# Optimization experiments

Measured on AMD Instinct MI355X. Metric: run time of the kernel, lower is better.

## Reference

```python
import jax, jax.numpy as jnp
import numpy as np

D_MODEL = 1024; D_STATE = 64; HEADDIM = 64; EXPAND = 2
D_INNER = EXPAND * D_MODEL            # 2048
NHEADS = D_INNER // HEADDIM           # 32
NGROUPS = 1
GN = NGROUPS * D_STATE                # 64
CONV_DIM = D_INNER + 2 * (2 * GN)     # 2304
D_IN_PROJ = 2 * D_INNER + 2 * (2 * GN) + 2 * NHEADS  # 4416
K_SP = 7; K_TP = 4; CHUNK = 256
BATCH = 2; FRAMES = 8; SPATIAL = 256; SEQLEN = SPATIAL * FRAMES  # 2048


def silu(x):
    return x * jax.nn.sigmoid(x)


def flip_frames(x, f):
    # 'b (l f) d -> b l f d' flip frame axis, flatten back
    b, L, d = x.shape
    return x.reshape(b, L // f, f, d)[:, :, ::-1, :].reshape(b, L, d)


def depthwise_conv1d(x, w, b, pad):
    # x: (N, L, C), w: (C, K) depthwise, pad=(lo,hi) -> (N, L_out, C)
    y = jax.lax.conv_general_dilated(
        jnp.transpose(x, (0, 2, 1)), w[:, None, :], (1,), [pad],
        feature_group_count=w.shape[0])
    return jnp.transpose(y + b[None, :, None], (0, 2, 1))


def setup_inputs():
    rng = np.random.default_rng(0)
    f32 = lambda *s: jnp.asarray(rng.standard_normal(s), jnp.float32)
    # dt_bias init exactly as in the torch module
    dt = np.exp(rng.random(NHEADS) * (np.log(0.1) - np.log(0.001)) + np.log(0.001))
    dt = np.clip(dt, 1e-4, None)
    inv_dt = dt + np.log(-np.expm1(-dt))
    return {
        "u": f32(BATCH, SEQLEN, D_MODEL),
        "in_proj_w": f32(D_IN_PROJ, D_MODEL) * 0.02,
        "conv_sp_w": f32(CONV_DIM, K_SP) * 0.2,
        "conv_sp_b": f32(CONV_DIM) * 0.02,
        "conv_tp_w": f32(CONV_DIM, K_TP) * 0.2,
        "conv_tp_b": f32(CONV_DIM) * 0.02,
        "dt_bias": jnp.asarray(inv_dt, jnp.float32),
        "A_log": jnp.zeros((NHEADS,), jnp.float32),
        "D": jnp.ones((NHEADS,), jnp.float32),
        "fc_D_w": f32(NHEADS, D_INNER) * 0.02,
        "norm_w": jnp.ones((D_INNER,), jnp.float32),
        "out_proj_w": f32(D_MODEL, D_INNER) * 0.02,
        "num_frames": FRAMES,
    }


def chunked_scan(xh, dt, A, Bm, Cm, sp, cs):
    # xh:(R,L,h,p) dt:(R,L,h) Bm,Cm:(R,L,n). ngroups=1.
    # seq_idx semantics: rows [0:b) one segment; rows [b:2b) reset every sp tokens.
    R, L, H, P = xh.shape
    nch = L // cs
    b = R // 2
    xch = xh.reshape(R, nch, cs, H, P)
    dtc = jnp.transpose(dt.reshape(R, nch, cs, H), (0, 1, 3, 2))   # (R,nch,h,cs)
    Bch = Bm.reshape(R, nch, cs, D_STATE)
    Cch = Cm.reshape(R, nch, cs, D_STATE)
    a = dtc * A[None, None, :, None]                               # negative logs
    cum = jnp.cumsum(a, axis=-1)                                   # inclusive
    mask = jnp.tril(jnp.ones((cs, cs), bool))
    seg = cum[..., :, None] - cum[..., None, :]                    # (R,nch,h,t,s)
    Lmat = jnp.where(mask, jnp.exp(jnp.where(mask, seg, 0.0)), 0.0)
    CB = jnp.einsum('rctn,rcsn->rcts', Cch, Bch)
    M = CB[:, :, None] * Lmat * dtc[:, :, :, None, :]
    Y_intra = jnp.einsum('rchts,rcshp->rcthp', M, xch)
    # chunk-final states and cross-chunk recurrence
    G = jnp.exp(cum[..., -1:] - cum) * dtc                         # (R,nch,h,cs)
    S_chunk = jnp.einsum('rchs,rcshp,rcsn->rchpn', G, xch, Bch)
    chunk_decay = jnp.exp(cum[..., -1])                            # (R,nch,h)
    cidx = jnp.arange(nch)
    rb = (cidx > 0) & ((cidx * cs) % sp == 0)
    resetc = jnp.concatenate([jnp.zeros((b, nch), bool),
                              jnp.broadcast_to(rb, (b, nch))], axis=0)

    def cstep(S, inp):
        dec, Sc, r = inp
        S = jnp.where(r[:, None, None, None], 0.0, S)
        prev = S
        S = dec[:, :, None, None] * S + Sc
        return S, prev

    S0 = jnp.zeros((R, H, P, D_STATE), xh.dtype)
    _, prevs = jax.lax.scan(
        cstep, S0,
        (jnp.transpose(chunk_decay, (1, 0, 2)),
         jnp.transpose(S_chunk, (1, 0, 2, 3, 4)),
         resetc.T))
    prev_states = jnp.transpose(prevs, (1, 0, 2, 3, 4))            # (R,nch,h,p,n)
    Y_inter = jnp.einsum('rcht,rctn,rchpn->rcthp', jnp.exp(cum), Cch, prev_states)
    return (Y_intra + Y_inter).reshape(R, L, H, P)


def reference(u, in_proj_w, conv_sp_w, conv_sp_b, conv_tp_w, conv_tp_b,
              dt_bias, A_log, D, fc_D_w, norm_w, out_proj_w, num_frames):
    batch, seqlen, _ = u.shape
    f = num_frames
    sp = seqlen // f
    zxbcdt = u @ in_proj_w.T
    z = zxbcdt[..., :D_INNER]
    xBC = zxbcdt[..., D_INNER:D_INNER + CONV_DIM]
    dt_raw = zxbcdt[..., D_INNER + CONV_DIM:]
    dt = jnp.concatenate([dt_raw[..., :NHEADS],
                          flip_frames(dt_raw[..., NHEADS:], f)], axis=0)
    dt = jax.nn.softplus(dt + dt_bias)                             # (2b,L,h)
    A = -jnp.exp(A_log)
    # spatial depthwise conv over spatial dim per frame ('same' pad) + SiLU
    xBC = xBC.reshape(batch, sp, f, CONV_DIM).transpose(0, 2, 1, 3).reshape(batch * f, sp, CONV_DIM)
    xBC = silu(depthwise_conv1d(xBC, conv_sp_w, conv_sp_b, (K_SP // 2, K_SP // 2)))
    # causal temporal depthwise conv over frame dim per spatial location + SiLU
    xBC = xBC.reshape(batch, f, sp, CONV_DIM).transpose(0, 2, 1, 3).reshape(batch * sp, f, CONV_DIM)
    xBC = silu(depthwise_conv1d(xBC, conv_tp_w, conv_tp_b, (K_TP - 1, 0)))
    xBC = xBC.reshape(batch, seqlen, CONV_DIM)
    x = xBC[..., :D_INNER]
    BC = xBC[..., D_INNER:]
    x_orig = x
    x2 = jnp.concatenate([x, flip_frames(x, f)], axis=0)
    BC2 = jnp.concatenate([BC[..., :2 * GN], flip_frames(BC[..., 2 * GN:], f)], axis=0)
    Bm, Cm = BC2[..., :GN], BC2[..., GN:]
    xh = x2.reshape(2 * batch, seqlen, NHEADS, HEADDIM)
    y = chunked_scan(xh, dt, A, Bm, Cm, sp, CHUNK)                 # (2b,L,h,p)
    y_fwd = y[:batch].reshape(batch, seqlen, D_INNER)
    y_rev = y[batch:].reshape(batch, sp, f, D_INNER)
    # roll-by-one with zeroed first position (fwd: token axis, rev: spatial axis)
    y_fwd = jnp.concatenate([jnp.zeros_like(y_fwd[:, :1]), y_fwd[:, :-1]], axis=1)
    y_rev = jnp.concatenate([jnp.zeros_like(y_rev[:, :1]), y_rev[:, :-1]], axis=1)
    y_rev = y_rev[:, :, ::-1, :].reshape(batch, seqlen, D_INNER)
    x_res = x_orig * jnp.repeat(x_orig @ fc_D_w.T + D, HEADDIM, axis=-1)
    y = y_fwd + y_rev + x_res
    # gated RMSNorm (norm_before_gate=True): rmsnorm(y)*w*silu(z)
    y = y * jax.lax.rsqrt(jnp.mean(jnp.square(y), axis=-1, keepdims=True) + 1e-5)
    y = y * norm_w * silu(z)
    return y @ out_proj_w.T
```

## Files before the change

kernel.cpp:

```cpp
#include <hip/hip_runtime.h>
#include <hip/hip_bf16.h>
#include <math.h>

#define D_STATE   64
#define HEADDIM   64
#define D_INNER   2048
#define NHEADS    32
#define GN        64
#define CONV_DIM  2304
#define D_IN_PROJ 4416
#define ZLD       4352
#define K_SP      7
#define K_TP      4
#define CHUNK     256
#define BATCHN    2
#define FRAMES    8
#define SPATIAL   256
#define SEQLEN    2048
#define NCH       8
#define MTOT      4096

typedef __attribute__((ext_vector_type(8))) short short8;
typedef __attribute__((ext_vector_type(8))) unsigned short ushort8v;
typedef __attribute__((ext_vector_type(4))) float floatx4;

__device__ __forceinline__ float silu_f(float x) { return x / (1.f + __expf(-x)); }
__device__ __forceinline__ int flip_l(int l) { return (l & ~7) | (7 - (l & 7)); }
__device__ __forceinline__ unsigned short f2bf(float f) {
  unsigned int u = __float_as_uint(f);
  unsigned int r = (u + 0x7fffu + ((u >> 16) & 1u)) >> 16;
  return (unsigned short)r;
}
__device__ __forceinline__ float bf2f(unsigned short s) {
  return __uint_as_float(((unsigned int)s) << 16);
}
__device__ __forceinline__ unsigned int cvtpk_bf16(float lo, float hi) {
  unsigned int r;
  asm("v_cvt_pk_bf16_f32 %0, %1, %2" : "=v"(r) : "v"(lo), "v"(hi));
  return r;
}
typedef union { short8 v; unsigned int u[4]; } s8u;
__device__ __forceinline__ void gload_lds16(const unsigned short* g, unsigned short* l) {
  __builtin_amdgcn_global_load_lds((const __attribute__((address_space(1))) void*)g,
                                   (__attribute__((address_space(3))) void*)l, 16, 0, 0);
}

__global__ __launch_bounds__(256) void cast4_bf16_kernel(const float* __restrict__ a,
                                                         unsigned short* __restrict__ oa,
                                                         int na,
                                                         const float* __restrict__ b,
                                                         unsigned short* __restrict__ ob,
                                                         int nb,
                                                         const float* __restrict__ c,
                                                         unsigned short* __restrict__ oc,
                                                         int nc,
                                                         const float* __restrict__ d,
                                                         unsigned short* __restrict__ od) {
  int bid = blockIdx.x;
  const float* in;
  unsigned short* out;
  size_t blk;
  if (bid < na)                 { in = a; out = oa; blk = bid; }
  else if (bid < na + nb)       { in = b; out = ob; blk = bid - na; }
  else if (bid < na + nb + nc)  { in = c; out = oc; blk = bid - na - nb; }
  else                          { in = d; out = od; blk = bid - na - nb - nc; }
  size_t i = (blk * 256 + threadIdx.x) * 4;
  float4 v = *(const float4*)(in + i);
  ushort4 o;
  o.x = f2bf(v.x); o.y = f2bf(v.y); o.z = f2bf(v.z); o.w = f2bf(v.w);
  *(ushort4*)(out + i) = o;
}

__global__ __launch_bounds__(256) void gemm_bk64_bf16out(
    const unsigned short* __restrict__ A, int lda,
    const unsigned short* __restrict__ B, int ldb,
    unsigned short* __restrict__ C, int ldc, int K) {
  __shared__ unsigned short As[128 * 64];
  __shared__ unsigned short Bs[128 * 64];
  const int tid = threadIdx.x;
  const int lane = tid & 63;
  const int w = tid >> 6;
  const int bid = blockIdx.x;
  const int xcd = bid & 7;
  const int rp  = bid >> 3;
  const int px  = rp % 17;
  const int py  = rp / 17;
  const int m0 = ((xcd >> 1) * 8 + py) * 128;
  const int n0 = ((xcd & 1) * 17 + px) * 128;
  const int wm = (w >> 1) * 64;
  const int wn = (w & 1) * 64;
  const int lrow = lane >> 3;
  const int lperm = lane & 7;
  floatx4 acc[4][4] = {};
  for (int k0 = 0; k0 < K; k0 += 64) {
#pragma unroll
    for (int j = 0; j < 8; ++j) {
      int g = j * 4 + w;
      if (g < 16) {
        int row = g * 8 + lrow;
        int cg = (lperm ^ (row & 7)) * 8;
        gload_lds16(A + (size_t)(m0 + row) * lda + k0 + cg, &As[g * 512]);
      } else {
        int gb = g - 16;
        int row = gb * 8 + lrow;
        int cg = (lperm ^ (row & 7)) * 8;
        gload_lds16(B + (size_t)(n0 + row) * ldb + k0 + cg, &Bs[gb * 512]);
      }
    }
    __syncthreads();
    const int fr = lane & 15;
    const int kq = (lane >> 4) * 8;
#pragma unroll
    for (int kk = 0; kk < 64; kk += 32) {
      int u = (kk + kq) >> 3;
      short8 af[4], bfr[4];
#pragma unroll
      for (int i = 0; i < 4; ++i) {
        int row = wm + i * 16 + fr;
        af[i] = *(const short8*)&As[(row * 8 + (u ^ (row & 7))) * 8];
      }
#pragma unroll
      for (int j = 0; j < 4; ++j) {
        int row = wn + j * 16 + fr;
        bfr[j] = *(const short8*)&Bs[(row * 8 + (u ^ (row & 7))) * 8];
      }
#pragma unroll
      for (int i = 0; i < 4; ++i)
#pragma unroll
        for (int j = 0; j < 4; ++j)
          acc[i][j] = __builtin_amdgcn_mfma_f32_16x16x32_bf16(af[i], bfr[j], acc[i][j], 0, 0, 0);
    }
    __syncthreads();
  }
  const int fr = lane & 15;
  const int rg = (lane >> 4) * 4;
  unsigned short* Ew = &As[w * 1024];
  const int rr = lane >> 3;
  const int c8 = (lane & 7) * 8;
#pragma unroll
  for (int i = 0; i < 4; ++i) {
#pragma unroll
    for (int q = 0; q < 4; ++q)
#pragma unroll
      for (int j = 0; j < 4; ++j)
        Ew[(rg + q) * 64 + j * 16 + fr] = f2bf(acc[i][j][q]);
    ushort8v v0 = *(const ushort8v*)&Ew[rr * 64 + c8];
    ushort8v v1 = *(const ushort8v*)&Ew[(rr + 8) * 64 + c8];
    *(ushort8v*)(C + (size_t)(m0 + wm + i * 16 + rr) * ldc + n0 + wn + c8) = v0;
    *(ushort8v*)(C + (size_t)(m0 + wm + i * 16 + rr + 8) * ldc + n0 + wn + c8) = v1;
  }
}

__global__ __launch_bounds__(256) void gemm_m64_f32(
    const unsigned short* __restrict__ A, int lda,
    const unsigned short* __restrict__ B, int ldb,
    float* __restrict__ C, int ldc, int K) {
  __shared__ unsigned short As[64 * 64];
  __shared__ unsigned short Bs[128 * 64];
  const int tid = threadIdx.x;
  const int lane = tid & 63;
  const int w = tid >> 6;
  const int bid = blockIdx.x;
  const int xcd = bid & 7;
  const int q8  = bid >> 3;
  const int rsel = q8 >> 5;
  const int rp   = q8 & 31;
  const int reg  = xcd + 8 * rsel;
  const int m0 = ((reg >> 1) * 8 + (rp >> 2)) * 64;
  const int n0 = ((reg & 1) * 4 + (rp & 3)) * 128;
  const int wm = (w >> 1) * 32;
  const int wn = (w & 1) * 64;
  const int lrow = lane >> 3;
  const int lperm = lane & 7;
  floatx4 acc[2][4] = {};
  for (int k0 = 0; k0 < K; k0 += 64) {
#pragma unroll
    for (int j = 0; j < 6; ++j) {
      int g = j * 4 + w;
      if (g < 8) {
        int row = g * 8 + lrow;
        int cg = (lperm ^ (row & 7)) * 8;
        gload_lds16(A + (size_t)(m0 + row) * lda + k0 + cg, &As[g * 512]);
      } else {
        int gb = g - 8;
        int row = gb * 8 + lrow;
        int cg = (lperm ^ (row & 7)) * 8;
        gload_lds16(B + (size_t)(n0 + row) * ldb + k0 + cg, &Bs[gb * 512]);
      }
    }
    __syncthreads();
    const int fr = lane & 15;
    const int kq = (lane >> 4) * 8;
#pragma unroll
    for (int kk = 0; kk < 64; kk += 32) {
      int u = (kk + kq) >> 3;
      short8 af[2], bfr[4];
#pragma unroll
      for (int i = 0; i < 2; ++i) {
        int row = wm + i * 16 + fr;
        af[i] = *(const short8*)&As[(row * 8 + (u ^ (row & 7))) * 8];
      }
#pragma unroll
      for (int j = 0; j < 4; ++j) {
        int row = wn + j * 16 + fr;
        bfr[j] = *(const short8*)&Bs[(row * 8 + (u ^ (row & 7))) * 8];
      }
#pragma unroll
      for (int i = 0; i < 2; ++i)
#pragma unroll
        for (int j = 0; j < 4; ++j)
          acc[i][j] = __builtin_amdgcn_mfma_f32_16x16x32_bf16(af[i], bfr[j], acc[i][j], 0, 0, 0);
    }
    __syncthreads();
  }
  const int col = lane & 15;
  const int rg = (lane >> 4) * 4;
#pragma unroll
  for (int i = 0; i < 2; ++i)
#pragma unroll
    for (int j = 0; j < 4; ++j)
#pragma unroll
      for (int r = 0; r < 4; ++r)
        C[(size_t)(m0 + wm + i * 16 + rg + r) * ldc + (n0 + wn + j * 16 + col)] = acc[i][j][r];
}

__device__ __forceinline__ void ts_body_bf16(const unsigned short* __restrict__ A, int lda,
                                             const unsigned short* __restrict__ B, int ldb,
                                             float* __restrict__ C, int ldc, int N, int K,
                                             int m0, float* red) {
  const int tid = threadIdx.x;
  const int lane = tid & 63;
  const int w = tid >> 6;
  const int fr = lane & 15;
  const int kq = (lane >> 4) * 8;
  const int nt = N >> 4;
  const int kseg = K >> 2;
  const int k0 = w * kseg;
  floatx4 acc[4] = {};
  for (int k = k0; k < k0 + kseg; k += 32) {
    short8 af = *(const short8*)(A + (size_t)(m0 + fr) * lda + k + kq);
    for (int j = 0; j < nt; ++j) {
      short8 bf8 = *(const short8*)(B + (size_t)(j * 16 + fr) * ldb + k + kq);
      acc[j] = __builtin_amdgcn_mfma_f32_16x16x32_bf16(af, bf8, acc[j], 0, 0, 0);
    }
  }
  const int rg = (lane >> 4) * 4;
  for (int j = 0; j < nt; ++j)
#pragma unroll
    for (int q = 0; q < 4; ++q)
      red[w * 1024 + j * 256 + (rg + q) * 16 + fr] = acc[j][q];
  __syncthreads();
  const int entries = nt * 256;
  for (int e = tid; e < entries; e += 256) {
    float s = red[e] + red[1024 + e] + red[2048 + e] + red[3072 + e];
    int j = e >> 8, idx = e & 255, row = idx >> 4, col = idx & 15;
    C[(size_t)(m0 + row) * ldc + j * 16 + col] = s;
  }
}

__global__ __launch_bounds__(256) void gemm_ts_bf16(
    const unsigned short* __restrict__ A, int lda,
    const unsigned short* __restrict__ B, int ldb,
    float* __restrict__ C, int ldc, int N, int K) {
  __shared__ float red[4 * 1024];
  ts_body_bf16(A, lda, B, ldb, C, ldc, N, K, blockIdx.x * 16, red);
}

__global__ __launch_bounds__(256) void fused_dtconv_kernel(
    const float* __restrict__ DTraw, const float* __restrict__ dt_bias,
    const float* __restrict__ A_log, float* __restrict__ DTt, float* __restrict__ CUMS,
    const unsigned short* __restrict__ Zb, const float* __restrict__ wsp,
    const float* __restrict__ bsp, const float* __restrict__ wtp,
    const float* __restrict__ btp, unsigned short* __restrict__ XTb) {
  __shared__ __align__(16) char smem[32768];
  const int tid = threadIdx.x;
  if (blockIdx.x < 1024) {
    float* sc = (float*)smem;
    int idx = blockIdx.x * 256 + tid;
    int l  = idx & 2047;
    int rh = idx >> 11;
    int h  = rh & 31;
    int r  = rh >> 5;
    int bi = r & 1;
    int ls = (r < 2) ? l : flip_l(l);
    int ch = (r < 2) ? h : NHEADS + h;
    float raw = DTraw[((size_t)bi * SEQLEN + ls) * 64 + ch] + dt_bias[h];
    float dtv = (raw > 20.f) ? raw : log1pf(__expf(raw));
    DTt[idx] = dtv;
    float A = -__expf(A_log[h]);
    float run = dtv * A;
    sc[tid] = run;
    __syncthreads();
#pragma unroll
    for (int ofs = 1; ofs < 256; ofs <<= 1) {
      float add = (tid >= ofs) ? sc[tid - ofs] : 0.f;
      __syncthreads();
      run += add;
      sc[tid] = run;
      __syncthreads();
    }
    CUMS[idx] = run;
  } else {
    typedef float4 xsl_t[8][32];
    xsl_t* xsl = (xsl_t*)smem;
    int bid = blockIdx.x - 1024;
    const int bx = bid % 18;
    const int by = (bid / 18) & 31;
    const int bz = bid / 576;
    const int g  = tid & 31;
    const int fr = tid >> 5;
    const int c  = bx * 128 + g * 4;
    const int s0 = by * 8;
    const int bi = bz;
    float wsp_r[4][K_SP];
#pragma unroll
    for (int ch = 0; ch < 4; ++ch)
#pragma unroll
      for (int j = 0; j < K_SP; ++j) wsp_r[ch][j] = wsp[(c + ch) * K_SP + j];
    float4 bsp4 = *(const float4*)(bsp + c);
    float4 z[14];
#pragma unroll
    for (int i = 0; i < 14; ++i) {
      int ss = s0 - 3 + i;
      if (0 <= ss && ss < SPATIAL) {
        ushort4 v = *(const ushort4*)(Zb + ((size_t)bi * SEQLEN + (ss*8 + fr)) * ZLD + D_INNER + c);
        z[i] = make_float4(bf2f(v.x), bf2f(v.y), bf2f(v.z), bf2f(v.w));
      } else {
        z[i] = make_float4(0.f, 0.f, 0.f, 0.f);
      }
    }
#pragma unroll
    for (int so = 0; so < 8; ++so) {
      float4 a = bsp4;
#pragma unroll
      for (int j = 0; j < K_SP; ++j) {
        a.x += wsp_r[0][j] * z[so + j].x;
        a.y += wsp_r[1][j] * z[so + j].y;
        a.z += wsp_r[2][j] * z[so + j].z;
        a.w += wsp_r[3][j] * z[so + j].w;
      }
      a.x = silu_f(a.x); a.y = silu_f(a.y); a.z = silu_f(a.z); a.w = silu_f(a.w);
      xsl[fr][so][g] = a;
    }
    __syncthreads();
    float wtp_r[4][K_TP];
#pragma unroll
    for (int ch = 0; ch < 4; ++ch)
#pragma unroll
      for (int j = 0; j < K_TP; ++j) wtp_r[ch][j] = wtp[(c + ch) * K_TP + j];
    float4 btp4 = *(const float4*)(btp + c);
#pragma unroll
    for (int so = 0; so < 8; ++so) {
      float4 t = btp4;
#pragma unroll
      for (int j = 0; j < K_TP; ++j) {
        int ff = fr + j - (K_TP - 1);
        if (ff >= 0) {
          float4 xv = xsl[ff][so][g];
          t.x += wtp_r[0][j] * xv.x;
          t.y += wtp_r[1][j] * xv.y;
          t.z += wtp_r[2][j] * xv.z;
          t.w += wtp_r[3][j] * xv.w;
        }
      }
      ushort4 o;
      o.x = f2bf(silu_f(t.x)); o.y = f2bf(silu_f(t.y));
      o.z = f2bf(silu_f(t.z)); o.w = f2bf(silu_f(t.w));
      *(ushort4*)(XTb + ((size_t)bi * SEQLEN + ((s0 + so)*8 + fr)) * CONV_DIM + c) = o;
    }
  }
}

__global__ __launch_bounds__(256) void fused_post_kernel(
    const unsigned short* __restrict__ XTb, const float* __restrict__ DTt,
    const float* __restrict__ CUMS, float* __restrict__ CBs,
    float* __restrict__ SCH, const unsigned short* __restrict__ FCDWb,
    float* __restrict__ FCD) {
  __shared__ __align__(16) char smem[35840];
  const int tid = threadIdx.x;
  const int bidx = blockIdx.x;
  const int lane = tid & 63;
  const int w = tid >> 6;
  if (bidx < 512) {
    unsigned short* Xs = (unsigned short*)smem;
    unsigned short* Bsm = Xs + 64 * 136;
    float* gs = (float*)(Bsm + 64 * 136);
    int c = bidx & 7;
    int h = (bidx >> 3) & 31;
    int r = bidx >> 8;
    int bi = r;
    int rh = r * NHEADS + h;
    float cl = CUMS[(size_t)rh*SEQLEN + c*CHUNK + 255];
    gs[tid] = __expf(cl - CUMS[(size_t)rh*SEQLEN + c*CHUNK + tid]) * DTt[(size_t)rh*SEQLEN + c*CHUNK + tid];
    const int fr = lane & 15;
    const int kq = (lane >> 4) * 8;
    const int sr = tid >> 3;
    const int p0 = (tid & 7) * 8;
    const int swz = (tid & 7) << 3;
    floatx4 acc[4] = {};
    for (int half = 0; half < 2; ++half) {
      __syncthreads();
#pragma unroll
      for (int P = 0; P < 4; ++P) {
        int s = P * 32 + sr;
        int l = c*CHUNK + half*128 + s;
        const unsigned short* row = XTb + ((size_t)bi*SEQLEN + l)*CONV_DIM;
        ushort8v xv = *(const ushort8v*)(row + h*HEADDIM + p0);
        ushort8v bv = *(const ushort8v*)(row + D_INNER + p0);
        float g = gs[half*128 + s];
        int cswz = s ^ swz;
#pragma unroll
        for (int q = 0; q < 8; ++q) {
          Xs[(p0 + q) * 136 + cswz] = f2bf(g * bf2f(xv[q]));
          Bsm[(p0 + q) * 136 + cswz] = bv[q];
        }
      }
      __syncthreads();
#pragma unroll
      for (int sl = 0; sl < 4; ++sl) {
        int s0 = sl * 32;
        int Ra = w*16 + fr;
        short8 af = *(const short8*)&Xs[Ra * 136 + ((s0 + kq) ^ (((Ra >> 3) & 7) << 3))];
#pragma unroll
        for (int j = 0; j < 4; ++j) {
          int Rb = j*16 + fr;
          short8 bf8 = *(const short8*)&Bsm[Rb * 136 + ((s0 + kq) ^ (((Rb >> 3) & 7) << 3))];
          acc[j] = __builtin_amdgcn_mfma_f32_16x16x32_bf16(af, bf8, acc[j], 0, 0, 0);
        }
      }
    }
    const int col = lane & 15;
    const int rg = (lane >> 4) * 4;
    size_t base = (((size_t)r*NCH + c)*NHEADS + h) * (size_t)(HEADDIM*D_STATE);
#pragma unroll
    for (int j = 0; j < 4; ++j)
#pragma unroll
      for (int q = 0; q < 4; ++q)
        SCH[base + (size_t)(w*16 + rg + q)*D_STATE + j*16 + col] = acc[j][q];
  } else if (bidx < 832) {
    const int TT0[10] = {0,1,1,2,2,2,3,3,3,3};
    const int SS0[10] = {0,0,1,0,1,2,0,1,2,3};
    int t = bidx - 512;
    int tt = t % 10;
    int rc = t / 10;
    int c = rc & 7;
    int r = rc >> 3;
    int t0 = TT0[tt] * 64;
    int s0 = SS0[tt] * 64;
    int bi = r & 1;
    int bOff = D_INNER + ((r < 2) ? 0 : 2*GN);
    int cOff = bOff + GN;
    const int fr = lane & 15;
    const int kq = (lane >> 4) * 8;
    int Lc = c * CHUNK + t0 + w * 16 + fr;
    if (r >= 2) Lc = flip_l(Lc);
    const unsigned short* crow = XTb + ((size_t)bi*SEQLEN + Lc)*CONV_DIM + cOff;
    short8 af0 = *(const short8*)(crow + kq);
    short8 af1 = *(const short8*)(crow + 32 + kq);
    floatx4 acc[4] = {};
#pragma unroll
    for (int j = 0; j < 4; ++j) {
      int Ls = c * CHUNK + s0 + j * 16 + fr;
      if (r >= 2) Ls = flip_l(Ls);
      const unsigned short* brow = XTb + ((size_t)bi*SEQLEN + Ls)*CONV_DIM + bOff;
      short8 bf0 = *(const short8*)(brow + kq);
      short8 bf1 = *(const short8*)(brow + 32 + kq);
      acc[j] = __builtin_amdgcn_mfma_f32_16x16x32_bf16(af0, bf0, acc[j], 0, 0, 0);
      acc[j] = __builtin_amdgcn_mfma_f32_16x16x32_bf16(af1, bf1, acc[j], 0, 0, 0);
    }
    const int col = lane & 15;
    const int rg = (lane >> 4) * 4;
    size_t base = (((size_t)r*NCH + c) * CHUNK) * CHUNK;
#pragma unroll
    for (int j = 0; j < 4; ++j)
#pragma unroll
      for (int q = 0; q < 4; ++q)
        CBs[base + (size_t)(t0 + w*16 + rg + q)*CHUNK + (s0 + j*16 + col)] = acc[j][q];
  } else {
    ts_body_bf16(XTb, CONV_DIM, FCDWb, 2048, FCD, 32, 32, 2048,
                 (bidx - 832) * 16, (float*)smem);
  }
}

__global__ __launch_bounds__(256) void state_combine_kernel(const float* __restrict__ SCH,
                                                            const float* __restrict__ CUMS,
                                                            float* __restrict__ SPREV) {
  int bid = blockIdx.x;
  int pq = bid & 3;
  int h = (bid >> 2) & 31;
  int r = bid >> 7;
  int tid = threadIdx.x;
  int p = pq*16 + (tid >> 4);
  int n = (tid & 15) * 4;
  float4 S = make_float4(0.f, 0.f, 0.f, 0.f);
  for (int c = 0; c < NCH; ++c) {
    size_t off = ((((size_t)r*NCH + c)*NHEADS + h)*HEADDIM + p)*D_STATE + n;
    *(float4*)(SPREV + off) = S;
    float dec = __expf(CUMS[((size_t)r*NHEADS + h)*SEQLEN + c*CHUNK + 255]);
    float4 v = *(const float4*)(SCH + off);
    S.x = dec*S.x + v.x; S.y = dec*S.y + v.y;
    S.z = dec*S.z + v.z; S.w = dec*S.w + v.w;
  }
}

#define YS_ED(S0)                                                              \
  float edv[8];                                                                \
  { float4 e0_ = *(const float4*)&ecd[(S0) + kq];                              \
    float4 e1_ = *(const float4*)&ecd[(S0) + kq + 4];                          \
    edv[0]=e0_.x; edv[1]=e0_.y; edv[2]=e0_.z; edv[3]=e0_.w;                    \
    edv[4]=e1_.x; edv[5]=e1_.y; edv[6]=e1_.z; edv[7]=e1_.w; }

#define YS_BFR(S0)                                                             \
  short8 bfr[4];                                                               \
  _Pragma("unroll")                                                            \
  for (int j = 0; j < 4; ++j) {                                                \
    int R = j * 16 + fr;                                                       \
    bfr[j] = *(const short8*)&Xt[R * 264 + (((S0) + kq) ^ (((R >> 3) & 7) << 3))]; \
  }

#define YS_MFMA4(AF, ACCROW)                                                   \
  _Pragma("unroll")                                                            \
  for (int j = 0; j < 4; ++j)                                                  \
    ACCROW[j] = __builtin_amdgcn_mfma_f32_16x16x32_bf16(AF, bfr[j], ACCROW[j], 0, 0, 0);

#define YS_AF_NOMASK(C0, C1, E)                                                \
  { af_.u[0] = cvtpk_bf16(C0.x*(E)*edv[0], C0.y*(E)*edv[1]);                   \
    af_.u[1] = cvtpk_bf16(C0.z*(E)*edv[2], C0.w*(E)*edv[3]);                   \
    af_.u[2] = cvtpk_bf16(C1.x*(E)*edv[4], C1.y*(E)*edv[5]);                   \
    af_.u[3] = cvtpk_bf16(C1.z*(E)*edv[6], C1.w*(E)*edv[7]); }

#define YS_AF_MASK(C0, C1, E, TROW)                                            \
  { float wz[8] = {C0.x,C0.y,C0.z,C0.w,C1.x,C1.y,C1.z,C1.w};                   \
    _Pragma("unroll")                                                          \
    for (int jj = 0; jj < 8; ++jj) {                                           \
      float t_ = wz[jj]*(E)*edv[jj];                                           \
      wz[jj] = (kq + jj <= (TROW)) ? t_ : 0.f; }                               \
    af_.u[0]=cvtpk_bf16(wz[0],wz[1]); af_.u[1]=cvtpk_bf16(wz[2],wz[3]);        \
    af_.u[2]=cvtpk_bf16(wz[4],wz[5]); af_.u[3]=cvtpk_bf16(wz[6],wz[7]); }

#define YS_STRIP(KS, E2, ACC)                                                  \
  {                                                                            \
    const int t0s_ = (KS) * 32;                                                \
    const float* cbr0 = CBs + cbbase + (size_t)(t0s_ + fr) * CHUNK + kq;       \
    const float* cbr1 = cbr0 + (size_t)16 * CHUNK;                             \
    float4 a0 = *(const float4*)cbr0;                                          \
    float4 a1 = *(const float4*)(cbr0 + 4);                                    \
    float4 b0 = *(const float4*)cbr1;                                          \
    float4 b1 = *(const float4*)(cbr1 + 4);                                    \
    for (int sl = 0; sl < (KS); ++sl) {                                        \
      int s0 = sl * 32;                                                        \
      float4 na0 = *(const float4*)(cbr0 + s0 + 32);                           \
      float4 na1 = *(const float4*)(cbr0 + s0 + 36);                           \
      float4 nb0 = *(const float4*)(cbr1 + s0 + 32);                           \
      float4 nb1 = *(const float4*)(cbr1 + s0 + 36);                           \
      YS_ED(s0); YS_BFR(s0);                                                   \
      s8u af_;                                                                 \
      YS_AF_NOMASK(a0, a1, (E2)[0]);                                           \
      YS_MFMA4(af_.v, ACC[0]);                                                 \
      YS_AF_NOMASK(b0, b1, (E2)[1]);                                           \
      YS_MFMA4(af_.v, ACC[1]);                                                 \
      a0 = na0; a1 = na1; b0 = nb0; b1 = nb1;                                  \
    }                                                                          \
    {                                                                          \
      int s0 = (KS) * 32;                                                      \
      YS_ED(s0); YS_BFR(s0);                                                   \
      s8u af_;                                                                 \
      YS_AF_MASK(a0, a1, (E2)[0], fr);                                         \
      YS_MFMA4(af_.v, ACC[0]);                                                 \
      YS_AF_MASK(b0, b1, (E2)[1], 16 + fr);                                    \
      YS_MFMA4(af_.v, ACC[1]);                                                 \
    }                                                                          \
  }

#define YS_INTER(T0S, E2, ACC)                                                 \
  _Pragma("unroll")                                                            \
  for (int i = 0; i < 2; ++i) {                                                \
    int t = (T0S) + i * 16 + fr;                                               \
    const unsigned short* crow = XTb + ((size_t)bi*SEQLEN + c*CHUNK + t)*CONV_DIM + D_INNER + GN + n0 + kq; \
    ushort4 c0 = *(const ushort4*)crow;                                        \
    ushort4 c1 = *(const ushort4*)(crow + 4);                                  \
    float eI = (E2)[i];                                                        \
    s8u af_;                                                                   \
    af_.u[0] = cvtpk_bf16(bf2f(c0.x)*eI, bf2f(c0.y)*eI);                       \
    af_.u[1] = cvtpk_bf16(bf2f(c0.z)*eI, bf2f(c0.w)*eI);                       \
    af_.u[2] = cvtpk_bf16(bf2f(c1.x)*eI, bf2f(c1.y)*eI);                       \
    af_.u[3] = cvtpk_bf16(bf2f(c1.z)*eI, bf2f(c1.w)*eI);                       \
    YS_MFMA4(af_.v, ACC[i]);                                                   \
  }

#define YS_EPI(T0S, ACC)                                                       \
  _Pragma("unroll")                                                            \
  for (int i = 0; i < 2; ++i) {                                                \
    _Pragma("unroll")                                                          \
    for (int q = 0; q < 4; ++q)                                                \
      _Pragma("unroll")                                                        \
      for (int j = 0; j < 4; ++j)                                              \
        Ew[(rg + q) * 64 + j * 16 + fr] = f2bf(ACC[i][j][q]);                  \
    ushort8v v0 = *(const ushort8v*)&Ew[rr * 64 + c8];                         \
    ushort8v v1 = *(const ushort8v*)&Ew[(rr + 8) * 64 + c8];                   \
    *(ushort8v*)(Yb16 + ybase + (size_t)((T0S) + i*16 + rr) * D_INNER + c8) = v0;      \
    *(ushort8v*)(Yb16 + ybase + (size_t)((T0S) + i*16 + rr + 8) * D_INNER + c8) = v1;  \
  }

__global__ __launch_bounds__(256, 4) void yscan_kernel(const unsigned short* __restrict__ XTb,
                                                       const float* __restrict__ DTt,
                                                       const float* __restrict__ CUMS,
                                                       const float* __restrict__ CBs,
                                                       const float* __restrict__ SPREV,
                                                       unsigned short* __restrict__ Yb16) {
  __shared__ unsigned short Xt[64 * 264];
  __shared__ float cums[CHUNK];
  __shared__ float ecd[CHUNK];
  int tid = threadIdx.x;
  int lane = tid & 63;
  int w = tid >> 6;
  int id = blockIdx.x;
  int c = id & 7;
  int h = (id >> 3) & 31;
  int r = id >> 8;
  int rh = r * NHEADS + h;
  int bi = r & 1;
  {
    int sr = tid >> 3;
    int p0 = (tid & 7) * 8;
    int swz = (tid & 7) << 3;
#pragma unroll
    for (int P = 0; P < 8; ++P) {
      int s = P * 32 + sr;
      int L = c * CHUNK + s;
      if (r >= 2) L = flip_l(L);
      ushort8v v = *(const ushort8v*)(XTb + ((size_t)bi * SEQLEN + L) * CONV_DIM + h * HEADDIM + p0);
      int cswz = s ^ swz;
#pragma unroll
      for (int q = 0; q < 8; ++q)
        Xt[(p0 + q) * 264 + cswz] = v[q];
    }
    float cv = CUMS[(size_t)rh * SEQLEN + c * CHUNK + tid];
    cums[tid] = cv;
    ecd[tid] = __expf(-cv) * DTt[(size_t)rh * SEQLEN + c * CHUNK + tid];
  }
  __syncthreads();
  const int fr = lane & 15;
  const int kq = (lane >> 4) * 8;
  const int kA = w, kB = 7 - w;
  const int tA = kA * 32, tB = kB * 32;
  float eAr[2], eBr[2];
#pragma unroll
  for (int i = 0; i < 2; ++i) {
    eAr[i] = __expf(cums[tA + i * 16 + fr]);
    eBr[i] = __expf(cums[tB + i * 16 + fr]);
  }
  floatx4 accA[2][4] = {};
  floatx4 accB[2][4] = {};
  size_t cbbase = (((size_t)r * NCH + c) * CHUNK) * CHUNK;
  YS_STRIP(kA, eAr, accA);
  YS_STRIP(kB, eBr, accB);
  if (r < 2) {
    const float* spbase = SPREV + (((size_t)r*NCH + c)*NHEADS + h) * (size_t)(HEADDIM*D_STATE);
#pragma unroll
    for (int ns = 0; ns < 2; ++ns) {
      int n0 = ns * 32;
      short8 bfr[4];
#pragma unroll
      for (int j = 0; j < 4; ++j) {
        const float* sp = spbase + (size_t)(j*16 + fr)*D_STATE + n0 + kq;
        float4 s0v = *(const float4*)sp;
        float4 s1v = *(const float4*)(sp + 4);
        s8u bb;
        bb.u[0] = cvtpk_bf16(s0v.x, s0v.y);
        bb.u[1] = cvtpk_bf16(s0v.z, s0v.w);
        bb.u[2] = cvtpk_bf16(s1v.x, s1v.y);
        bb.u[3] = cvtpk_bf16(s1v.z, s1v.w);
        bfr[j] = bb.v;
      }
      YS_INTER(tA, eAr, accA);
      YS_INTER(tB, eBr, accB);
    }
  }
  __syncthreads();
  unsigned short* Ew = Xt + w * 1024;
  const int rg = (lane >> 4) * 4;
  const int rr = lane >> 3;
  const int c8 = (lane & 7) * 8;
  size_t ybase = ((size_t)r*SEQLEN + c*CHUNK)*D_INNER + h*HEADDIM;
  YS_EPI(tA, accA);
  YS_EPI(tB, accB);
}

__global__ __launch_bounds__(256) void combine_kernel(const unsigned short* __restrict__ Y,
                                                      const unsigned short* __restrict__ XTb,
                                                      const float* __restrict__ FCD,
                                                      const float* __restrict__ Dp,
                                                      const unsigned short* __restrict__ Zb,
                                                      const float* __restrict__ norm_w,
                                                      unsigned short* __restrict__ YPb) {
  __shared__ float red4[4];
  int row = blockIdx.x;
  int bi = row >> 11;
  int l = row & 2047;
  int s = l >> 3, fr = l & 7;
  int tid = threadIdx.x;
  int d0 = tid * 8;
  const unsigned short* yf = (l >= 1) ? Y + ((size_t)bi*SEQLEN + (l-1))*D_INNER + d0 : nullptr;
  const unsigned short* yr = (s >= 1) ? Y + ((size_t)(2+bi)*SEQLEN + ((s-1)*8 + (7-fr)))*D_INNER + d0 : nullptr;
  const unsigned short* xr = XTb + ((size_t)row)*CONV_DIM + d0;
  float fcv = FCD[(size_t)row*NHEADS + (d0 >> 6)] + Dp[d0 >> 6];
  ushort8v xv8 = *(const ushort8v*)xr;
  float v[8];
#pragma unroll
  for (int q = 0; q < 8; ++q) v[q] = bf2f(xv8[q]) * fcv;
  if (yf) {
    ushort8v a = *(const ushort8v*)yf;
#pragma unroll
    for (int q = 0; q < 8; ++q) v[q] += bf2f(a[q]);
  }
  if (yr) {
    ushort8v a = *(const ushort8v*)yr;
#pragma unroll
    for (int q = 0; q < 8; ++q) v[q] += bf2f(a[q]);
  }
  float ss = 0.f;
#pragma unroll
  for (int q = 0; q < 8; ++q) ss += v[q] * v[q];
#pragma unroll
  for (int d = 1; d < 64; d <<= 1) ss += __shfl_xor(ss, d, 64);
  if ((tid & 63) == 0) red4[tid >> 6] = ss;
  __syncthreads();
  float tot = red4[0] + red4[1] + red4[2] + red4[3];
  float rs = rsqrtf(tot / (float)D_INNER + 1e-5f);
  ushort8v zv8 = *(const ushort8v*)(Zb + ((size_t)row)*ZLD + d0);
  float4 nw0 = *(const float4*)(norm_w + d0);
  float4 nw1 = *(const float4*)(norm_w + d0 + 4);
  float nw[8] = {nw0.x,nw0.y,nw0.z,nw0.w,nw1.x,nw1.y,nw1.z,nw1.w};
  ushort8v o;
#pragma unroll
  for (int q = 0; q < 8; ++q)
    o[q] = f2bf(v[q] * rs * nw[q] * silu_f(bf2f(zv8[q])));
  *(ushort8v*)(YPb + (size_t)row*D_INNER + d0) = o;
}

extern "C" void kernel_launch(void* const* d_in, const int* in_sizes, int n_in,
                              void* d_out, int out_size, void* d_ws, size_t ws_size,
                              hipStream_t stream) {
  (void)in_sizes; (void)n_in; (void)out_size; (void)ws_size;
  const float* u          = (const float*)d_in[0];
  const float* in_proj_w  = (const float*)d_in[1];
  const float* conv_sp_w  = (const float*)d_in[2];
  const float* conv_sp_b  = (const float*)d_in[3];
  const float* conv_tp_w  = (const float*)d_in[4];
  const float* conv_tp_b  = (const float*)d_in[5];
  const float* dt_bias    = (const float*)d_in[6];
  const float* A_log      = (const float*)d_in[7];
  const float* Dp         = (const float*)d_in[8];
  const float* fc_D_w     = (const float*)d_in[9];
  const float* norm_w     = (const float*)d_in[10];
  const float* out_proj_w = (const float*)d_in[11];
  float* out = (float*)d_out;
  float* ws = (float*)d_ws;

  float* Z     = ws;
  float* SH    = Z     + 17825792ULL;
  float* XT    = SH    + 9437184ULL;
  float* DTt   = XT    + 9437184ULL;
  float* Yb    = DTt   + 262144ULL;
  float* SPREV = Yb    + 16777216ULL;
  float* FCD   = SPREV + 2097152ULL;
  float* DTraw = FCD   + 131072ULL;
  float* CUMS  = DTraw + 262144ULL;

  unsigned short* Zb   = (unsigned short*)Z;
  unsigned short* XTb  = (unsigned short*)XT;
  unsigned short* Yb16 = (unsigned short*)Yb;
  unsigned short* Ub   = (unsigned short*)Yb;
  unsigned short* Wb   = (unsigned short*)Yb + 4194304ULL;
  float* SCH = Yb + 8388608ULL;
  unsigned short* Wob = (unsigned short*)(Yb + 10485760ULL);
  unsigned short* FCDWb = (unsigned short*)(Yb + 11534336ULL);
  unsigned short* YPb = (unsigned short*)SH;

  cast4_bf16_kernel<<<10624, 256, 0, stream>>>(u, Ub, 4096, in_proj_w, Wb, 4416,
                                               out_proj_w, Wob, 2048, fc_D_w, FCDWb);
  gemm_bk64_bf16out<<<dim3(1088), 256, 0, stream>>>(Ub, 1024, Wb, 1024, Zb, ZLD, 1024);
  gemm_ts_bf16<<<256, 256, 0, stream>>>(Ub, 1024, Wb + 4352ULL*1024, 1024,
                                        DTraw, 64, 64, 1024);
  fused_dtconv_kernel<<<2176, 256, 0, stream>>>(DTraw, dt_bias, A_log, DTt, CUMS,
                                                Zb, conv_sp_w, conv_sp_b,
                                                conv_tp_w, conv_tp_b, XTb);
  fused_post_kernel<<<1088, 256, 0, stream>>>(XTb, DTt, CUMS, SH, SCH, FCDWb, FCD);
  state_combine_kernel<<<256, 256, 0, stream>>>(SCH, CUMS, SPREV);
  yscan_kernel<<<dim3(1024), 256, 0, stream>>>(XTb, DTt, CUMS, SH, SPREV, Yb16);
  combine_kernel<<<4096, 256, 0, stream>>>(Yb16, XTb, FCD, Dp, Zb, norm_w, YPb);
  gemm_m64_f32<<<dim3(512), 256, 0, stream>>>(YPb, 2048, Wob, 2048, out, 1024, 2048);
}
```

Measured before the change: 289.9 us.

## Fuse dt GEMM into main GEMM and inline state combine into yscan

```diff
diff --git a/kernel.cpp b/kernel.cpp
--- a/kernel.cpp
+++ b/kernel.cpp
@@ -71,15 +71,56 @@
   *(ushort4*)(out + i) = o;
 }
 
-__global__ __launch_bounds__(256) void gemm_bk64_bf16out(
-    const unsigned short* __restrict__ A, int lda,
-    const unsigned short* __restrict__ B, int ldb,
-    unsigned short* __restrict__ C, int ldc, int K) {
-  __shared__ unsigned short As[128 * 64];
-  __shared__ unsigned short Bs[128 * 64];
+__device__ __forceinline__ void ts_body_bf16(const unsigned short* __restrict__ A, int lda,
+                                             const unsigned short* __restrict__ B, int ldb,
+                                             float* __restrict__ C, int ldc, int N, int K,
+                                             int m0, float* red) {
   const int tid = threadIdx.x;
   const int lane = tid & 63;
   const int w = tid >> 6;
+  const int fr = lane & 15;
+  const int kq = (lane >> 4) * 8;
+  const int nt = N >> 4;
+  const int kseg = K >> 2;
+  const int k0 = w * kseg;
+  floatx4 acc[4] = {};
+  for (int k = k0; k < k0 + kseg; k += 32) {
+    short8 af = *(const short8*)(A + (size_t)(m0 + fr) * lda + k + kq);
+    for (int j = 0; j < nt; ++j) {
+      short8 bf8 = *(const short8*)(B + (size_t)(j * 16 + fr) * ldb + k + kq);
+      acc[j] = __builtin_amdgcn_mfma_f32_16x16x32_bf16(af, bf8, acc[j], 0, 0, 0);
+    }
+  }
+  const int rg = (lane >> 4) * 4;
+  for (int j = 0; j < nt; ++j)
+#pragma unroll
+    for (int q = 0; q < 4; ++q)
+      red[w * 1024 + j * 256 + (rg + q) * 16 + fr] = acc[j][q];
+  __syncthreads();
+  const int entries = nt * 256;
+  for (int e = tid; e < entries; e += 256) {
+    float s = red[e] + red[1024 + e] + red[2048 + e] + red[3072 + e];
+    int j = e >> 8, idx = e & 255, row = idx >> 4, col = idx & 15;
+    C[(size_t)(m0 + row) * ldc + j * 16 + col] = s;
+  }
+}
+
+__global__ __launch_bounds__(256) void gemm_main_kernel(
+    const unsigned short* __restrict__ A, int lda,
+    const unsigned short* __restrict__ B, int ldb,
+    unsigned short* __restrict__ C, int ldc, int K,
+    const unsigned short* __restrict__ Bdt, float* __restrict__ DTraw) {
+  __shared__ __align__(16) char smem[32768];
+  const int tid = threadIdx.x;
+  const int lane = tid & 63;
+  const int w = tid >> 6;
+  if (blockIdx.x >= 1088) {
+    ts_body_bf16(A, lda, Bdt, lda, DTraw, 64, 64, K,
+                 (blockIdx.x - 1088) * 16, (float*)smem);
+    return;
+  }
+  unsigned short* As = (unsigned short*)smem;
+  unsigned short* Bs = As + 128 * 64;
   const int bid = blockIdx.x;
   const int xcd = bid & 7;
   const int rp  = bid >> 3;
@@ -222,48 +263,6 @@
 #pragma unroll
       for (int r = 0; r < 4; ++r)
         C[(size_t)(m0 + wm + i * 16 + rg + r) * ldc + (n0 + wn + j * 16 + col)] = acc[i][j][r];
-}
-
-__device__ __forceinline__ void ts_body_bf16(const unsigned short* __restrict__ A, int lda,
-                                             const unsigned short* __restrict__ B, int ldb,
-                                             float* __restrict__ C, int ldc, int N, int K,
-                                             int m0, float* red) {
-  const int tid = threadIdx.x;
-  const int lane = tid & 63;
-  const int w = tid >> 6;
-  const int fr = lane & 15;
-  const int kq = (lane >> 4) * 8;
-  const int nt = N >> 4;
-  const int kseg = K >> 2;
-  const int k0 = w * kseg;
-  floatx4 acc[4] = {};
-  for (int k = k0; k < k0 + kseg; k += 32) {
-    short8 af = *(const short8*)(A + (size_t)(m0 + fr) * lda + k + kq);
-    for (int j = 0; j < nt; ++j) {
-      short8 bf8 = *(const short8*)(B + (size_t)(j * 16 + fr) * ldb + k + kq);
-      acc[j] = __builtin_amdgcn_mfma_f32_16x16x32_bf16(af, bf8, acc[j], 0, 0, 0);
-    }
-  }
-  const int rg = (lane >> 4) * 4;
-  for (int j = 0; j < nt; ++j)
-#pragma unroll
-    for (int q = 0; q < 4; ++q)
-      red[w * 1024 + j * 256 + (rg + q) * 16 + fr] = acc[j][q];
-  __syncthreads();
-  const int entries = nt * 256;
-  for (int e = tid; e < entries; e += 256) {
-    float s = red[e] + red[1024 + e] + red[2048 + e] + red[3072 + e];
-    int j = e >> 8, idx = e & 255, row = idx >> 4, col = idx & 15;
-    C[(size_t)(m0 + row) * ldc + j * 16 + col] = s;
-  }
-}
-
-__global__ __launch_bounds__(256) void gemm_ts_bf16(
-    const unsigned short* __restrict__ A, int lda,
-    const unsigned short* __restrict__ B, int ldb,
-    float* __restrict__ C, int ldc, int N, int K) {
-  __shared__ float red[4 * 1024];
-  ts_body_bf16(A, lda, B, ldb, C, ldc, N, K, blockIdx.x * 16, red);
 }
 
 __global__ __launch_bounds__(256) void fused_dtconv_kernel(
@@ -440,11 +439,11 @@
   } else if (bidx < 832) {
     const int TT0[10] = {0,1,1,2,2,2,3,3,3,3};
     const int SS0[10] = {0,0,1,0,1,2,0,1,2,3};
-    int t = bidx - 512;
-    int tt = t % 10;
-    int rc = t / 10;
-    int c = rc & 7;
-    int r = rc >> 3;
+    int idx = bidx - 512;
+    int c = idx & 7;
+    int k = idx >> 3;
+    int tt = k % 10;
+    int r = k / 10;
     int t0 = TT0[tt] * 64;
     int s0 = SS0[tt] * 64;
     int bi = r & 1;
@@ -479,27 +478,6 @@
   } else {
     ts_body_bf16(XTb, CONV_DIM, FCDWb, 2048, FCD, 32, 32, 2048,
                  (bidx - 832) * 16, (float*)smem);
-  }
-}
-
-__global__ __launch_bounds__(256) void state_combine_kernel(const float* __restrict__ SCH,
-                                                            const float* __restrict__ CUMS,
-                                                            float* __restrict__ SPREV) {
-  int bid = blockIdx.x;
-  int pq = bid & 3;
-  int h = (bid >> 2) & 31;
-  int r = bid >> 7;
-  int tid = threadIdx.x;
-  int p = pq*16 + (tid >> 4);
-  int n = (tid & 15) * 4;
-  float4 S = make_float4(0.f, 0.f, 0.f, 0.f);
-  for (int c = 0; c < NCH; ++c) {
-    size_t off = ((((size_t)r*NCH + c)*NHEADS + h)*HEADDIM + p)*D_STATE + n;
-    *(float4*)(SPREV + off) = S;
-    float dec = __expf(CUMS[((size_t)r*NHEADS + h)*SEQLEN + c*CHUNK + 255]);
-    float4 v = *(const float4*)(SCH + off);
-    S.x = dec*S.x + v.x; S.y = dec*S.y + v.y;
-    S.z = dec*S.z + v.z; S.w = dec*S.w + v.w;
   }
 }
 
@@ -606,7 +584,7 @@
                                                        const float* __restrict__ DTt,
                                                        const float* __restrict__ CUMS,
                                                        const float* __restrict__ CBs,
-                                                       const float* __restrict__ SPREV,
+                                                       const float* __restrict__ SCH,
                                                        unsigned short* __restrict__ Yb16) {
   __shared__ unsigned short Xt[64 * 264];
   __shared__ float cums[CHUNK];
@@ -653,30 +631,41 @@
   floatx4 accA[2][4] = {};
   floatx4 accB[2][4] = {};
   size_t cbbase = (((size_t)r * NCH + c) * CHUNK) * CHUNK;
+  if (r < 2) {
+#pragma unroll
+    for (int ns = 0; ns < 2; ++ns) {
+      int n0 = ns * 32;
+      float sp[4][8] = {};
+      for (int cp = 0; cp < c; ++cp) {
+        float dec = __expf(CUMS[(size_t)rh*SEQLEN + cp*CHUNK + 255]);
+        const float* sb = SCH + (((size_t)r*NCH + cp)*NHEADS + h) * (size_t)(HEADDIM*D_STATE);
+#pragma unroll
+        for (int j = 0; j < 4; ++j) {
+          const float* p = sb + (size_t)(j*16 + fr)*D_STATE + n0 + kq;
+          float4 v0 = *(const float4*)p;
+          float4 v1 = *(const float4*)(p + 4);
+          sp[j][0] = dec*sp[j][0] + v0.x; sp[j][1] = dec*sp[j][1] + v0.y;
+          sp[j][2] = dec*sp[j][2] + v0.z; sp[j][3] = dec*sp[j][3] + v0.w;
+          sp[j][4] = dec*sp[j][4] + v1.x; sp[j][5] = dec*sp[j][5] + v1.y;
+          sp[j][6] = dec*sp[j][6] + v1.z; sp[j][7] = dec*sp[j][7] + v1.w;
+        }
+      }
+      short8 bfr[4];
+#pragma unroll
+      for (int j = 0; j < 4; ++j) {
+        s8u bb;
+        bb.u[0] = cvtpk_bf16(sp[j][0], sp[j][1]);
+        bb.u[1] = cvtpk_bf16(sp[j][2], sp[j][3]);
+        bb.u[2] = cvtpk_bf16(sp[j][4], sp[j][5]);
+        bb.u[3] = cvtpk_bf16(sp[j][6], sp[j][7]);
+        bfr[j] = bb.v;
+      }
+      YS_INTER(tA, eAr, accA);
+      YS_INTER(tB, eBr, accB);
+    }
+  }
   YS_STRIP(kA, eAr, accA);
   YS_STRIP(kB, eBr, accB);
-  if (r < 2) {
-    const float* spbase = SPREV + (((size_t)r*NCH + c)*NHEADS + h) * (size_t)(HEADDIM*D_STATE);
-#pragma unroll
-    for (int ns = 0; ns < 2; ++ns) {
-      int n0 = ns * 32;
-      short8 bfr[4];
-#pragma unroll
-      for (int j = 0; j < 4; ++j) {
-        const float* sp = spbase + (size_t)(j*16 + fr)*D_STATE + n0 + kq;
-        float4 s0v = *(const float4*)sp;
-        float4 s1v = *(const float4*)(sp + 4);
-        s8u bb;
-        bb.u[0] = cvtpk_bf16(s0v.x, s0v.y);
-        bb.u[1] = cvtpk_bf16(s0v.z, s0v.w);
-        bb.u[2] = cvtpk_bf16(s1v.x, s1v.y);
-        bb.u[3] = cvtpk_bf16(s1v.z, s1v.w);
-        bfr[j] = bb.v;
-      }
-      YS_INTER(tA, eAr, accA);
-      YS_INTER(tB, eBr, accB);
-    }
-  }
   __syncthreads();
   unsigned short* Ew = Xt + w * 1024;
   const int rg = (lane >> 4) * 4;
@@ -780,15 +769,13 @@
 
   cast4_bf16_kernel<<<10624, 256, 0, stream>>>(u, Ub, 4096, in_proj_w, Wb, 4416,
                                                out_proj_w, Wob, 2048, fc_D_w, FCDWb);
-  gemm_bk64_bf16out<<<dim3(1088), 256, 0, stream>>>(Ub, 1024, Wb, 1024, Zb, ZLD, 1024);
-  gemm_ts_bf16<<<256, 256, 0, stream>>>(Ub, 1024, Wb + 4352ULL*1024, 1024,
-                                        DTraw, 64, 64, 1024);
+  gemm_main_kernel<<<dim3(1344), 256, 0, stream>>>(Ub, 1024, Wb, 1024, Zb, ZLD, 1024,
+                                                   Wb + 4352ULL*1024, DTraw);
   fused_dtconv_kernel<<<2176, 256, 0, stream>>>(DTraw, dt_bias, A_log, DTt, CUMS,
                                                 Zb, conv_sp_w, conv_sp_b,
                                                 conv_tp_w, conv_tp_b, XTb);
   fused_post_kernel<<<1088, 256, 0, stream>>>(XTb, DTt, CUMS, SH, SCH, FCDWb, FCD);
-  state_combine_kernel<<<256, 256, 0, stream>>>(SCH, CUMS, SPREV);
-  yscan_kernel<<<dim3(1024), 256, 0, stream>>>(XTb, DTt, CUMS, SH, SPREV, Yb16);
+  yscan_kernel<<<dim3(1024), 256, 0, stream>>>(XTb, DTt, CUMS, SH, SCH, Yb16);
   combine_kernel<<<4096, 256, 0, stream>>>(Yb16, XTb, FCD, Dp, Zb, norm_w, YPb);
   gemm_m64_f32<<<dim3(512), 256, 0, stream>>>(YPb, 2048, Wob, 2048, out, 1024, 2048);
 }
```

Result: slower. 302.3 us (+4.3%).
